# Kernel optimization log

Hardware: AMD Instinct MI355X
Metric: run time of the kernel (lower is better)

The kernel has to match this reference:

```python
import math
import jax, jax.numpy as jnp
import numpy as np

NUM_CLASSES = 15
GAUSSIAN_FACTOR = 12.0
SCORE_THRESHOLD = 0.23
EPS = 1e-9
IMG = 1024
STRIDES = [8, 16, 32, 64, 128]
REGRESS_RANGES = [(-1.0, 64.0), (64.0, 128.0), (128.0, 256.0), (256.0, 512.0), (512.0, 1e8)]
NUM_ANCHORS_PER_LEVEL = [(IMG // s) ** 2 for s in STRIDES]
RANGES_PER_ANCHOR = np.concatenate(
    [np.tile(np.array(r, np.float32), (n, 1)) for r, n in zip(REGRESS_RANGES, NUM_ANCHORS_PER_LEVEL)], axis=0)


def rbox_to_poly(rb):
    # rb: (..., 5) [cx, cy, w, h, angle] -> (..., 4, 2) corners
    cx, cy, w, h, ang = (rb[..., 0], rb[..., 1], rb[..., 2], rb[..., 3], rb[..., 4])
    cxs = jnp.stack([-w / 2, w / 2, w / 2, -w / 2], axis=-1)
    cys = jnp.stack([-h / 2, -h / 2, h / 2, h / 2], axis=-1)
    ca = jnp.cos(ang)[..., None]
    sa = jnp.sin(ang)[..., None]
    px = cxs * ca - cys * sa + cx[..., None]
    py = cxs * sa + cys * ca + cy[..., None]
    return jnp.stack([px, py], axis=-1)


def rbox_to_gauss(rb):
    # rbox -> 2D gaussian (mean, covariance entries a, b, c)
    x, y, w, h, a = (rb[..., 0], rb[..., 1], rb[..., 2], rb[..., 3], rb[..., 4])
    ca, sa = jnp.cos(a), jnp.sin(a)
    w2, h2 = w * w / 12.0, h * h / 12.0
    return x, y, w2 * ca * ca + h2 * sa * sa, w2 * sa * sa + h2 * ca * ca, (w2 - h2) * ca * sa


def probiou(box1, box2, eps=1e-3):
    # ProbIoU between rotated boxes via Bhattacharyya distance of gaussians
    x1, y1, a1, b1, c1 = rbox_to_gauss(box1)
    x2, y2, a2, b2, c2 = rbox_to_gauss(box2)
    dx, dy = x1 - x2, y1 - y2
    aa, bb, cc = a1 + a2, b1 + b2, c1 + c2
    denom = aa * bb - cc * cc + eps
    t1 = 0.25 * (aa * dy * dy + bb * dx * dx) / denom
    t2 = 0.5 * (cc * (-dx) * dy) / denom
    det1 = jnp.maximum(a1 * b1 - c1 * c1, 0.0)
    det2 = jnp.maximum(a2 * b2 - c2 * c2, 0.0)
    t3 = 0.5 * jnp.log(denom / (4.0 * jnp.sqrt(det1 * det2) + eps) + eps)
    bd = jnp.clip(t1 + t2 + t3, eps, 100.0)
    return 1.0 - jnp.sqrt(1.0 - jnp.exp(-bd) + eps)


def _forward(pred_scores, pred_boxes, anchor_points, gt_labels, gt_boxes, pad_gt_mask, bg_index, stride_tensor):
    B, L, C = pred_scores.shape
    polys = rbox_to_poly(gt_boxes)                        # (B,N,4,2)
    a = polys[..., 0, :]
    b = polys[..., 1, :]
    d = polys[..., 3, :]
    vab = b - a                                           # (B,N,2)
    vad = d - a
    pts = anchor_points[None]                             # (1,1,L,2)
    # ---- gaussian distribution scores ----
    ctp = pts - gt_boxes[:, :, None, :2]                  # (B,N,L,2)
    dot_ab = jnp.sum(ctp * vab[:, :, None, :], -1)        # (B,N,L)
    dot_ad = jnp.sum(ctp * vad[:, :, None, :], -1)
    norm_ab = jnp.sqrt(jnp.sum(vab * vab, -1) + EPS)[:, :, None]
    norm_ad = jnp.sqrt(jnp.sum(vad * vad, -1) + EPS)[:, :, None]
    min_edge = jnp.min(gt_boxes[..., 2:4], -1)[:, :, None]
    delta_x = dot_ab ** 2 / (norm_ab ** 3 * min_edge + EPS)
    delta_y = dot_ad ** 2 / (norm_ad ** 3 * min_edge + EPS)
    gauss = jnp.exp(-0.5 * GAUSSIAN_FACTOR * (delta_x + delta_y))
    sigma = min_edge / GAUSSIAN_FACTOR
    refined = gauss / (2.0 * math.pi * sigma + EPS)
    # ---- geometric constraints: inside rotated polygon AND score > threshold ----
    ap = pts - a[:, :, None, :]                           # (B,N,L,2)
    ap_ab = jnp.sum(ap * vab[:, :, None, :], -1)
    ap_ad = jnp.sum(ap * vad[:, :, None, :], -1)
    nab2 = jnp.sum(vab * vab, -1)[:, :, None]
    nad2 = jnp.sum(vad * vad, -1)[:, :, None]
    inside = (ap_ab >= EPS) & (ap_ab <= nab2) & (ap_ad >= EPS) & (ap_ad <= nad2)
    inside_mask = (inside & (gauss > SCORE_THRESHOLD)).astype(pred_scores.dtype)
    # ---- multi-level range constraint on axis-aligned hull ----
    cx, cy, w, h, ang = (gt_boxes[..., i] for i in range(5))
    ca, sa = jnp.abs(jnp.cos(ang)), jnp.abs(jnp.sin(ang))
    ew = 0.5 * (w * ca + h * sa)
    eh = 0.5 * (w * sa + h * ca)
    x1y1 = jnp.stack([cx - ew, cy - eh], -1)[:, :, None, :]
    x2y2 = jnp.stack([cx + ew, cy + eh], -1)[:, :, None, :]
    ltrb_max = jnp.maximum(jnp.max(pts - x1y1, -1), jnp.max(x2y2 - pts, -1))  # (B,N,L)
    rr = jnp.asarray(RANGES_PER_ANCHOR)                   # (L,2)
    low = rr[None, None, :, 0]
    high = rr[None, None, :, 1]
    range_mask = ((ltrb_max >= low) & (ltrb_max <= high)).astype(pred_scores.dtype)
    # ---- combine masks and select best GT per anchor ----
    positive_mask = inside_mask * range_mask * pad_gt_mask  # (B,N,L), pad (B,N,1)
    masked = refined * positive_mask - (1.0 - positive_mask)
    best_idx = jnp.argmax(masked, axis=1)                 # (B,L)
    best_score = jnp.max(masked, axis=1)
    pos = best_score > 0.0
    lbl = jnp.take_along_axis(gt_labels[..., 0], best_idx, axis=1)
    assigned_labels = jnp.where(pos, lbl, bg_index)
    gb = jnp.take_along_axis(gt_boxes, best_idx[..., None], axis=1)  # (B,L,5)
    assigned_boxes = jnp.where(pos[..., None], gb, 0.0)
    # ---- IoU-weighted one-hot quality scores ----
    oh = jax.nn.one_hot(assigned_labels, NUM_CLASSES + 1, dtype=pred_scores.dtype)
    oh = jnp.delete(oh, bg_index, axis=-1)                # drop background column
    iou = jnp.where(pos, probiou(pred_boxes, gb), 0.0)
    assigned_scores = oh * iou[..., None]
    return assigned_labels, assigned_boxes, assigned_scores


def setup_inputs() -> dict:
    key = jax.random.key(0)
    ks = jax.random.split(key, 6)
    pts, strides = [], []
    for s in STRIDES:
        n = IMG // s
        xs = (np.arange(n, dtype=np.float32) + 0.5) * s
        gy, gx = np.meshgrid(xs, xs, indexing='ij')
        pts.append(np.stack([gx.ravel(), gy.ravel()], -1))
        strides.append(np.full((n * n, 1), float(s), np.float32))
    anchor_points = jnp.asarray(np.concatenate(pts, 0))[None]       # (1,L,2)
    stride_tensor = jnp.asarray(np.concatenate(strides, 0))[None]   # (1,L,1)
    L = anchor_points.shape[1]
    B, N, C = 8, 64, NUM_CLASSES

    def rand_rboxes(k, shape):
        k1, k2, k3 = jax.random.split(k, 3)
        cxy = jax.random.uniform(k1, shape[:-1] + (2,), minval=0.0, maxval=float(IMG))
        wh = jax.random.uniform(k2, shape[:-1] + (2,), minval=16.0, maxval=256.0)
        ang = jax.random.uniform(k3, shape[:-1] + (1,), minval=-np.pi / 2, maxval=np.pi / 2)
        return jnp.concatenate([cxy, wh, ang], -1).astype(jnp.float32)

    return {
        'pred_scores': jax.nn.sigmoid(jax.random.normal(ks[0], (B, L, C), jnp.float32)),
        'pred_boxes': rand_rboxes(ks[1], (B, L, 5)),
        'anchor_points': anchor_points,
        'gt_labels': jax.random.randint(ks[2], (B, N, 1), 0, C),
        'gt_boxes': rand_rboxes(ks[3], (B, N, 5)),
        'pad_gt_mask': jnp.ones((B, N, 1), jnp.float32),
        'bg_index': C,
        'stride_tensor': stride_tensor,
    }


def reference(pred_scores, pred_boxes, anchor_points, gt_labels, gt_boxes, pad_gt_mask, bg_index, stride_tensor):
    return _forward(pred_scores, pred_boxes, anchor_points, gt_labels, gt_boxes, pad_gt_mask, bg_index, stride_tensor)
```

## Files before the change

### kernel.cpp

```cpp
#include <hip/hip_runtime.h>
#include <math.h>


#define NUMC 15
#define NGT  64
#define LTOT 21824
#define NB   8
#define EPSV 1e-9f
#define SCORE_THR 0.23f

__global__ __launch_bounds__(256) void rga_main(
    const float* __restrict__ pred_boxes,
    const float* __restrict__ anchor_points,
    const int*   __restrict__ gt_labels,
    const float* __restrict__ gt_boxes,
    const float* __restrict__ pad_gt_mask,
    const int*   __restrict__ bg_index_p,
    float* __restrict__ out)
{
    __shared__ float4 SA[NGT][5];
    __shared__ float4 SE[NGT][2];

    const int b   = blockIdx.y;
    const int tid = threadIdx.x;

    if (tid < NGT) {
        const float* g = gt_boxes + (size_t)(b * NGT + tid) * 5;
        const float cx = g[0], cy = g[1], w = g[2], h = g[3], ang = g[4];
        const float ca = cosf(ang), sa = sinf(ang);
        const float hw = 0.5f * w, hh = 0.5f * h;
        const float ax = (-hw) * ca - (-hh) * sa + cx;
        const float ay = (-hw) * sa + (-hh) * ca + cy;
        const float bx = ( hw) * ca - (-hh) * sa + cx;
        const float by = ( hw) * sa + (-hh) * ca + cy;
        const float dx_ = (-hw) * ca - ( hh) * sa + cx;
        const float dy_ = (-hw) * sa + ( hh) * ca + cy;
        const float vabx = bx - ax, vaby = by - ay;
        const float vadx = dx_ - ax, vady = dy_ - ay;
        const float nab2 = vabx * vabx + vaby * vaby;
        const float nad2 = vadx * vadx + vady * vady;
        const float norm_ab = sqrtf(nab2 + EPSV);
        const float norm_ad = sqrtf(nad2 + EPSV);
        const float min_edge = fminf(w, h);
        const float inv_dxden = 1.0f / (norm_ab * norm_ab * norm_ab * min_edge + EPSV);
        const float inv_dyden = 1.0f / (norm_ad * norm_ad * norm_ad * min_edge + EPSV);
        const float sigma = min_edge / 12.0f;
        const float inv_refden = 1.0f / (6.2831853071795864769f * sigma + EPSV);
        const float aca = fabsf(ca), asa = fabsf(sa);
        const float ew = 0.5f * (w * aca + h * asa);
        const float eh = 0.5f * (w * asa + h * aca);
        const float w2 = w * w / 12.0f, h2 = h * h / 12.0f;
        const float ga2 = w2 * ca * ca + h2 * sa * sa;
        const float gb2 = w2 * sa * sa + h2 * ca * ca;
        const float gc2 = (w2 - h2) * ca * sa;
        const float det2 = fmaxf(ga2 * gb2 - gc2 * gc2, 0.0f);
        const float labelf = (float)gt_labels[b * NGT + tid];
        const float pad    = pad_gt_mask[b * NGT + tid];

        SA[tid][0] = make_float4(cx, cy, ax, ay);
        SA[tid][1] = make_float4(vabx, vaby, vadx, vady);
        SA[tid][2] = make_float4(nab2, nad2, inv_dxden, inv_dyden);
        SA[tid][3] = make_float4(cx - ew, cy - eh, cx + ew, cy + eh);
        SA[tid][4] = make_float4(inv_refden, pad, labelf, 0.0f);
        SE[tid][0] = make_float4(w, h, ang, det2);
        SE[tid][1] = make_float4(ga2, gb2, gc2, 0.0f);
    }
    __syncthreads();

    const int l = blockIdx.x * blockDim.x + tid;
    if (l >= LTOT) return;

    const float2 p = ((const float2*)anchor_points)[l];
    const float px = p.x, py = p.y;

    float low, high;
    if (l < 16384)      { low = -1.0f;   high = 64.0f;  }
    else if (l < 20480) { low = 64.0f;   high = 128.0f; }
    else if (l < 21504) { low = 128.0f;  high = 256.0f; }
    else if (l < 21760) { low = 256.0f;  high = 512.0f; }
    else                { low = 512.0f;  high = 1e8f;   }

    float best = -2.0f;
    int   bidx = 0;
    #pragma unroll 4
    for (int n = 0; n < NGT; ++n) {
        const float4 f0 = SA[n][0];
        const float4 f1 = SA[n][1];
        const float4 f2 = SA[n][2];
        const float4 f3 = SA[n][3];
        const float4 f4 = SA[n][4];
        const float ctpx = px - f0.x, ctpy = py - f0.y;
        const float dot_ab = ctpx * f1.x + ctpy * f1.y;
        const float dot_ad = ctpx * f1.z + ctpy * f1.w;
        const float delta = dot_ab * dot_ab * f2.z + dot_ad * dot_ad * f2.w;
        const float gauss = expf(-6.0f * delta);
        const float apx = px - f0.z, apy = py - f0.w;
        const float ap_ab = apx * f1.x + apy * f1.y;
        const float ap_ad = apx * f1.z + apy * f1.w;
        const bool inside = (ap_ab >= EPSV) & (ap_ab <= f2.x) &
                            (ap_ad >= EPSV) & (ap_ad <= f2.y);
        const float ltrb = fmaxf(fmaxf(px - f3.x, py - f3.y),
                                 fmaxf(f3.z - px, f3.w - py));
        const bool ok = inside & (gauss > SCORE_THR) & (ltrb >= low) & (ltrb <= high);
        const float mask = ok ? f4.y : 0.0f;
        const float masked = gauss * f4.x * mask - (1.0f - mask);
        if (masked > best) { best = masked; bidx = n; }
    }

    const int bg = bg_index_p[0];
    const bool pos = best > 0.0f;

    const float4 s0 = SA[bidx][0];
    const float4 s4 = SA[bidx][4];
    const float4 e0 = SE[bidx][0];
    const float4 e1 = SE[bidx][1];

    const int lbl = pos ? (int)s4.z : bg;

    const size_t idx = (size_t)b * LTOT + l;
    out[idx] = (float)lbl;

    float* outB = out + (size_t)NB * LTOT + idx * 5;
    outB[0] = pos ? s0.x : 0.0f;
    outB[1] = pos ? s0.y : 0.0f;
    outB[2] = pos ? e0.x : 0.0f;
    outB[3] = pos ? e0.y : 0.0f;
    outB[4] = pos ? e0.z : 0.0f;

    float iou = 0.0f;
    if (pos) {
        const float* pb = pred_boxes + idx * 5;
        const float pcx = pb[0], pcy = pb[1], pw = pb[2], ph = pb[3], pang = pb[4];
        const float ca = cosf(pang), sa = sinf(pang);
        const float w2 = pw * pw / 12.0f, h2 = ph * ph / 12.0f;
        const float a1 = w2 * ca * ca + h2 * sa * sa;
        const float b1 = w2 * sa * sa + h2 * ca * ca;
        const float c1 = (w2 - h2) * ca * sa;
        const float dx = pcx - s0.x, dy = pcy - s0.y;
        const float aa = a1 + e1.x, bb = b1 + e1.y, cc = c1 + e1.z;
        const float denom = aa * bb - cc * cc + 1e-3f;
        const float t1 = 0.25f * (aa * dy * dy + bb * dx * dx) / denom;
        const float t2 = 0.5f * (cc * (-(dx * dy))) / denom;
        const float det1 = fmaxf(a1 * b1 - c1 * c1, 0.0f);
        const float t3 = 0.5f * logf(denom / (4.0f * sqrtf(det1 * e0.w) + 1e-3f) + 1e-3f);
        float bd = t1 + t2 + t3;
        bd = fminf(fmaxf(bd, 1e-3f), 100.0f);
        iou = 1.0f - sqrtf(1.0f - expf(-bd) + 1e-3f);
    }

    float* outS = out + (size_t)NB * LTOT * 6 + idx * NUMC;
    #pragma unroll
    for (int c = 0; c < NUMC; ++c)
        outS[c] = (pos && c == lbl) ? iou : 0.0f;
}

extern "C" void kernel_launch(void* const* d_in, const int* in_sizes, int n_in,
                              void* d_out, int out_size, void* d_ws, size_t ws_size,
                              hipStream_t stream) {
    const float* pred_boxes    = (const float*)d_in[1];
    const float* anchor_points = (const float*)d_in[2];
    const int*   gt_labels     = (const int*)d_in[3];
    const float* gt_boxes      = (const float*)d_in[4];
    const float* pad_gt_mask   = (const float*)d_in[5];
    const int*   bg_index_p    = (const int*)d_in[6];
    float*       out           = (float*)d_out;

    dim3 grid((LTOT + 255) / 256, NB);
    rga_main<<<grid, dim3(256), 0, stream>>>(
        pred_boxes, anchor_points, gt_labels, gt_boxes, pad_gt_mask, bg_index_p, out);
}
```

Before: 96.74 us.

## Precompute GT box features in separate kernel; read via uniform global loads

Moves the per-GT-box feature precomputation into a separate single-block prep kernel that writes to workspace. The main kernel now reads those features through uniform global (scalar-cacheable) loads instead of shared memory, which removes the per-block trig prologue and the block barrier. It also simplifies the masked-score expression with a fused multiply-add and switches to fast-math intrinsics for exp, log and trig. The trade-off is an extra kernel launch, plus small accuracy changes from the intrinsics.

```diff
diff --git a/kernel.cpp b/kernel.cpp
--- a/kernel.cpp
+++ b/kernel.cpp
@@ -9,65 +9,66 @@
 #define EPSV 1e-9f
 #define SCORE_THR 0.23f
 
+
+__global__ __launch_bounds__(512) void rga_prep(
+    const float* __restrict__ gt_boxes,
+    const int*   __restrict__ gt_labels,
+    const float* __restrict__ pad_gt_mask,
+    float4* __restrict__ W)
+{
+    const int t = threadIdx.x;
+    if (t >= NB * NGT) return;
+    const float* g = gt_boxes + (size_t)t * 5;
+    const float cx = g[0], cy = g[1], w = g[2], h = g[3], ang = g[4];
+    const float ca = cosf(ang), sa = sinf(ang);
+    const float hw = 0.5f * w, hh = 0.5f * h;
+    const float ax = (-hw) * ca - (-hh) * sa + cx;
+    const float ay = (-hw) * sa + (-hh) * ca + cy;
+    const float bx = ( hw) * ca - (-hh) * sa + cx;
+    const float by = ( hw) * sa + (-hh) * ca + cy;
+    const float dx_ = (-hw) * ca - ( hh) * sa + cx;
+    const float dy_ = (-hw) * sa + ( hh) * ca + cy;
+    const float vabx = bx - ax, vaby = by - ay;
+    const float vadx = dx_ - ax, vady = dy_ - ay;
+    const float nab2 = vabx * vabx + vaby * vaby;
+    const float nad2 = vadx * vadx + vady * vady;
+    const float norm_ab = sqrtf(nab2 + EPSV);
+    const float norm_ad = sqrtf(nad2 + EPSV);
+    const float min_edge = fminf(w, h);
+    const float inv_dxden = 1.0f / (norm_ab * norm_ab * norm_ab * min_edge + EPSV);
+    const float inv_dyden = 1.0f / (norm_ad * norm_ad * norm_ad * min_edge + EPSV);
+    const float sigma = min_edge / 12.0f;
+    const float inv_refden = 1.0f / (6.2831853071795864769f * sigma + EPSV);
+    const float aca = fabsf(ca), asa = fabsf(sa);
+    const float ew = 0.5f * (w * aca + h * asa);
+    const float eh = 0.5f * (w * asa + h * aca);
+    const float w2 = w * w / 12.0f, h2 = h * h / 12.0f;
+    const float ga2 = w2 * ca * ca + h2 * sa * sa;
+    const float gb2 = w2 * sa * sa + h2 * ca * ca;
+    const float gc2 = (w2 - h2) * ca * sa;
+    const float det2 = fmaxf(ga2 * gb2 - gc2 * gc2, 0.0f);
+    const float pad = pad_gt_mask[t];
+    const float labelf = (float)gt_labels[t];
+
+    float4* o = W + (size_t)t * 7;
+    o[0] = make_float4(cx, cy, ax, ay);
+    o[1] = make_float4(vabx, vaby, vadx, vady);
+    o[2] = make_float4(nab2, nad2, inv_dxden, inv_dyden);
+    o[3] = make_float4(cx - ew, cy - eh, cx + ew, cy + eh);
+    o[4] = make_float4(inv_refden * pad, pad - 1.0f, labelf, 0.0f);
+    o[5] = make_float4(w, h, ang, det2);
+    o[6] = make_float4(ga2, gb2, gc2, 0.0f);
+}
+
 __global__ __launch_bounds__(256) void rga_main(
-    const float* __restrict__ pred_boxes,
-    const float* __restrict__ anchor_points,
-    const int*   __restrict__ gt_labels,
-    const float* __restrict__ gt_boxes,
-    const float* __restrict__ pad_gt_mask,
-    const int*   __restrict__ bg_index_p,
+    const float*  __restrict__ pred_boxes,
+    const float*  __restrict__ anchor_points,
+    const int*    __restrict__ bg_index_p,
+    const float4* __restrict__ W,
     float* __restrict__ out)
 {
-    __shared__ float4 SA[NGT][5];
-    __shared__ float4 SE[NGT][2];
-
-    const int b   = blockIdx.y;
-    const int tid = threadIdx.x;
-
-    if (tid < NGT) {
-        const float* g = gt_boxes + (size_t)(b * NGT + tid) * 5;
-        const float cx = g[0], cy = g[1], w = g[2], h = g[3], ang = g[4];
-        const float ca = cosf(ang), sa = sinf(ang);
-        const float hw = 0.5f * w, hh = 0.5f * h;
-        const float ax = (-hw) * ca - (-hh) * sa + cx;
-        const float ay = (-hw) * sa + (-hh) * ca + cy;
-        const float bx = ( hw) * ca - (-hh) * sa + cx;
-        const float by = ( hw) * sa + (-hh) * ca + cy;
-        const float dx_ = (-hw) * ca - ( hh) * sa + cx;
-        const float dy_ = (-hw) * sa + ( hh) * ca + cy;
-        const float vabx = bx - ax, vaby = by - ay;
-        const float vadx = dx_ - ax, vady = dy_ - ay;
-        const float nab2 = vabx * vabx + vaby * vaby;
-        const float nad2 = vadx * vadx + vady * vady;
-        const float norm_ab = sqrtf(nab2 + EPSV);
-        const float norm_ad = sqrtf(nad2 + EPSV);
-        const float min_edge = fminf(w, h);
-        const float inv_dxden = 1.0f / (norm_ab * norm_ab * norm_ab * min_edge + EPSV);
-        const float inv_dyden = 1.0f / (norm_ad * norm_ad * norm_ad * min_edge + EPSV);
-        const float sigma = min_edge / 12.0f;
-        const float inv_refden = 1.0f / (6.2831853071795864769f * sigma + EPSV);
-        const float aca = fabsf(ca), asa = fabsf(sa);
-        const float ew = 0.5f * (w * aca + h * asa);
-        const float eh = 0.5f * (w * asa + h * aca);
-        const float w2 = w * w / 12.0f, h2 = h * h / 12.0f;
-        const float ga2 = w2 * ca * ca + h2 * sa * sa;
-        const float gb2 = w2 * sa * sa + h2 * ca * ca;
-        const float gc2 = (w2 - h2) * ca * sa;
-        const float det2 = fmaxf(ga2 * gb2 - gc2 * gc2, 0.0f);
-        const float labelf = (float)gt_labels[b * NGT + tid];
-        const float pad    = pad_gt_mask[b * NGT + tid];
-
-        SA[tid][0] = make_float4(cx, cy, ax, ay);
-        SA[tid][1] = make_float4(vabx, vaby, vadx, vady);
-        SA[tid][2] = make_float4(nab2, nad2, inv_dxden, inv_dyden);
-        SA[tid][3] = make_float4(cx - ew, cy - eh, cx + ew, cy + eh);
-        SA[tid][4] = make_float4(inv_refden, pad, labelf, 0.0f);
-        SE[tid][0] = make_float4(w, h, ang, det2);
-        SE[tid][1] = make_float4(ga2, gb2, gc2, 0.0f);
-    }
-    __syncthreads();
-
-    const int l = blockIdx.x * blockDim.x + tid;
+    const int b = blockIdx.y;
+    const int l = blockIdx.x * blockDim.x + threadIdx.x;
     if (l >= LTOT) return;
 
     const float2 p = ((const float2*)anchor_points)[l];
@@ -80,20 +81,22 @@
     else if (l < 21760) { low = 256.0f;  high = 512.0f; }
     else                { low = 512.0f;  high = 1e8f;   }
 
+    const float4* __restrict__ Pb = W + (size_t)b * NGT * 7;
+
     float best = -2.0f;
     int   bidx = 0;
-    #pragma unroll 4
+    #pragma unroll 2
     for (int n = 0; n < NGT; ++n) {
-        const float4 f0 = SA[n][0];
-        const float4 f1 = SA[n][1];
-        const float4 f2 = SA[n][2];
-        const float4 f3 = SA[n][3];
-        const float4 f4 = SA[n][4];
+        const float4 f0 = Pb[n * 7 + 0];
+        const float4 f1 = Pb[n * 7 + 1];
+        const float4 f2 = Pb[n * 7 + 2];
+        const float4 f3 = Pb[n * 7 + 3];
+        const float4 f4 = Pb[n * 7 + 4];
         const float ctpx = px - f0.x, ctpy = py - f0.y;
         const float dot_ab = ctpx * f1.x + ctpy * f1.y;
         const float dot_ad = ctpx * f1.z + ctpy * f1.w;
         const float delta = dot_ab * dot_ab * f2.z + dot_ad * dot_ad * f2.w;
-        const float gauss = expf(-6.0f * delta);
+        const float gauss = __expf(-6.0f * delta);
         const float apx = px - f0.z, apy = py - f0.w;
         const float ap_ab = apx * f1.x + apy * f1.y;
         const float ap_ad = apx * f1.z + apy * f1.w;
@@ -102,18 +105,18 @@
         const float ltrb = fmaxf(fmaxf(px - f3.x, py - f3.y),
                                  fmaxf(f3.z - px, f3.w - py));
         const bool ok = inside & (gauss > SCORE_THR) & (ltrb >= low) & (ltrb <= high);
-        const float mask = ok ? f4.y : 0.0f;
-        const float masked = gauss * f4.x * mask - (1.0f - mask);
+        const float masked = ok ? fmaf(gauss, f4.x, f4.y) : -1.0f;
         if (masked > best) { best = masked; bidx = n; }
     }
 
     const int bg = bg_index_p[0];
     const bool pos = best > 0.0f;
 
-    const float4 s0 = SA[bidx][0];
-    const float4 s4 = SA[bidx][4];
-    const float4 e0 = SE[bidx][0];
-    const float4 e1 = SE[bidx][1];
+    const float4* Wn = Pb + bidx * 7;
+    const float4 s0 = Wn[0];
+    const float4 s4 = Wn[4];
+    const float4 e0 = Wn[5];
+    const float4 e1 = Wn[6];
 
     const int lbl = pos ? (int)s4.z : bg;
 
@@ -131,7 +134,7 @@
     if (pos) {
         const float* pb = pred_boxes + idx * 5;
         const float pcx = pb[0], pcy = pb[1], pw = pb[2], ph = pb[3], pang = pb[4];
-        const float ca = cosf(pang), sa = sinf(pang);
+        const float ca = __cosf(pang), sa = __sinf(pang);
         const float w2 = pw * pw / 12.0f, h2 = ph * ph / 12.0f;
         const float a1 = w2 * ca * ca + h2 * sa * sa;
         const float b1 = w2 * sa * sa + h2 * ca * ca;
@@ -142,10 +145,10 @@
         const float t1 = 0.25f * (aa * dy * dy + bb * dx * dx) / denom;
         const float t2 = 0.5f * (cc * (-(dx * dy))) / denom;
         const float det1 = fmaxf(a1 * b1 - c1 * c1, 0.0f);
-        const float t3 = 0.5f * logf(denom / (4.0f * sqrtf(det1 * e0.w) + 1e-3f) + 1e-3f);
+        const float t3 = 0.5f * __logf(denom / (4.0f * __fsqrt_rn(det1 * e0.w) + 1e-3f) + 1e-3f);
         float bd = t1 + t2 + t3;
         bd = fminf(fmaxf(bd, 1e-3f), 100.0f);
-        iou = 1.0f - sqrtf(1.0f - expf(-bd) + 1e-3f);
+        iou = 1.0f - sqrtf(1.0f - __expf(-bd) + 1e-3f);
     }
 
     float* outS = out + (size_t)NB * LTOT * 6 + idx * NUMC;
@@ -164,8 +167,11 @@
     const float* pad_gt_mask   = (const float*)d_in[5];
     const int*   bg_index_p    = (const int*)d_in[6];
     float*       out           = (float*)d_out;
+    float4*      W             = (float4*)d_ws;
+
+    rga_prep<<<dim3(1), dim3(512), 0, stream>>>(gt_boxes, gt_labels, pad_gt_mask, W);
 
     dim3 grid((LTOT + 255) / 256, NB);
     rga_main<<<grid, dim3(256), 0, stream>>>(
-        pred_boxes, anchor_points, gt_labels, gt_boxes, pad_gt_mask, bg_index_p, out);
+        pred_boxes, anchor_points, bg_index_p, W, out);
 }
```

Measured after the change: 98.39 us. About the same (+1.7%).

## Cull GT boxes per block by spatial and range overlap before anchor loop

Applied to the files above, without the earlier changes.

Each block derives its pyramid level and row span from its block index, then builds a compacted list of GT boxes whose axis-aligned extent and size could match anchors in that tile. Only those boxes are scanned per anchor, which skips most of the 64-box loop. The change also switches to fast intrinsics (__expf, __sinf, __cosf, __logf) and folds the pad mask into a single fma. The risks are small numerical differences from the fast math and correctness depending on the culling margins being conservative.

```diff
diff --git a/kernel.cpp b/kernel.cpp
--- a/kernel.cpp
+++ b/kernel.cpp
@@ -8,8 +8,9 @@
 #define NB   8
 #define EPSV 1e-9f
 #define SCORE_THR 0.23f
-
-__global__ __launch_bounds__(256) void rga_main(
+#define MARG 2.0f
+
+__global__ __launch_bounds__(256) void rga_fused(
     const float* __restrict__ pred_boxes,
     const float* __restrict__ anchor_points,
     const int*   __restrict__ gt_labels,
@@ -20,22 +21,43 @@
 {
     __shared__ float4 SA[NGT][5];
     __shared__ float4 SE[NGT][2];
+    __shared__ int    keep_list[NGT];
+    __shared__ int    keep_cnt;
 
     const int b   = blockIdx.y;
+    const int bx  = blockIdx.x;
     const int tid = threadIdx.x;
 
+    int Ls, sgn, log2nc;
+    float low, high;
+    if (bx < 64)      { Ls = 0;     sgn = 8;   log2nc = 7; low = -1.0f;  high = 64.0f;  }
+    else if (bx < 80) { Ls = 16384; sgn = 16;  log2nc = 6; low = 64.0f;  high = 128.0f; }
+    else if (bx < 84) { Ls = 20480; sgn = 32;  log2nc = 5; low = 128.0f; high = 256.0f; }
+    else if (bx < 85) { Ls = 21504; sgn = 64;  log2nc = 4; low = 256.0f; high = 512.0f; }
+    else              { Ls = 21760; sgn = 128; log2nc = 3; low = 512.0f; high = 1e8f;   }
+    const int   nc     = 1 << log2nc;
+    const int   row0   = (bx * 256 - Ls) >> log2nc;
+    const int   nrows  = 256 >> log2nc;
+    const int   rowlast = min(row0 + nrows, nc) - 1;
+    const float fs     = (float)sgn;
+    const float bymin  = (row0 + 0.5f) * fs;
+    const float bymax  = (rowlast + 0.5f) * fs;
+    const float bxmin  = 0.5f * fs;
+    const float bxmax  = (nc - 0.5f) * fs;
+
     if (tid < NGT) {
-        const float* g = gt_boxes + (size_t)(b * NGT + tid) * 5;
+        const int gi = b * NGT + tid;
+        const float* g = gt_boxes + (size_t)gi * 5;
         const float cx = g[0], cy = g[1], w = g[2], h = g[3], ang = g[4];
         const float ca = cosf(ang), sa = sinf(ang);
         const float hw = 0.5f * w, hh = 0.5f * h;
         const float ax = (-hw) * ca - (-hh) * sa + cx;
         const float ay = (-hw) * sa + (-hh) * ca + cy;
-        const float bx = ( hw) * ca - (-hh) * sa + cx;
-        const float by = ( hw) * sa + (-hh) * ca + cy;
+        const float bx_ = ( hw) * ca - (-hh) * sa + cx;
+        const float by_ = ( hw) * sa + (-hh) * ca + cy;
         const float dx_ = (-hw) * ca - ( hh) * sa + cx;
         const float dy_ = (-hw) * sa + ( hh) * ca + cy;
-        const float vabx = bx - ax, vaby = by - ay;
+        const float vabx = bx_ - ax, vaby = by_ - ay;
         const float vadx = dx_ - ax, vady = dy_ - ay;
         const float nab2 = vabx * vabx + vaby * vaby;
         const float nad2 = vadx * vadx + vady * vady;
@@ -54,36 +76,44 @@
         const float gb2 = w2 * sa * sa + h2 * ca * ca;
         const float gc2 = (w2 - h2) * ca * sa;
         const float det2 = fmaxf(ga2 * gb2 - gc2 * gc2, 0.0f);
-        const float labelf = (float)gt_labels[b * NGT + tid];
-        const float pad    = pad_gt_mask[b * NGT + tid];
+        const float pad = pad_gt_mask[gi];
+        const float labelf = (float)gt_labels[gi];
+        const float x1 = cx - ew, y1 = cy - eh, x2 = cx + ew, y2 = cy + eh;
 
         SA[tid][0] = make_float4(cx, cy, ax, ay);
         SA[tid][1] = make_float4(vabx, vaby, vadx, vady);
         SA[tid][2] = make_float4(nab2, nad2, inv_dxden, inv_dyden);
-        SA[tid][3] = make_float4(cx - ew, cy - eh, cx + ew, cy + eh);
-        SA[tid][4] = make_float4(inv_refden, pad, labelf, 0.0f);
+        SA[tid][3] = make_float4(x1, y1, x2, y2);
+        SA[tid][4] = make_float4(inv_refden * pad, pad - 1.0f, labelf, 0.0f);
         SE[tid][0] = make_float4(w, h, ang, det2);
         SE[tid][1] = make_float4(ga2, gb2, gc2, 0.0f);
+
+        const float me = fmaxf(ew, eh);
+        const bool keep =
+            (x1 <= bxmax + MARG) && (x2 >= bxmin - MARG) &&
+            (y1 <= bymax + MARG) && (y2 >= bymin - MARG) &&
+            (me <= high + MARG) && (2.0f * me >= low - MARG) &&
+            (pad > 0.0f);
+        const unsigned long long bal = __ballot(keep);
+        const int lane = tid & 63;
+        const int pos_i = (int)__popcll(bal & ((1ULL << lane) - 1ULL));
+        if (keep) keep_list[pos_i] = tid;
+        if (lane == 0) keep_cnt = (int)__popcll(bal);
     }
     __syncthreads();
 
-    const int l = blockIdx.x * blockDim.x + tid;
-    if (l >= LTOT) return;
+    const int cnt = keep_cnt;
+    const int l_raw = bx * 256 + tid;
+    if (l_raw >= LTOT) return;
+    const int l = l_raw;
 
     const float2 p = ((const float2*)anchor_points)[l];
     const float px = p.x, py = p.y;
 
-    float low, high;
-    if (l < 16384)      { low = -1.0f;   high = 64.0f;  }
-    else if (l < 20480) { low = 64.0f;   high = 128.0f; }
-    else if (l < 21504) { low = 128.0f;  high = 256.0f; }
-    else if (l < 21760) { low = 256.0f;  high = 512.0f; }
-    else                { low = 512.0f;  high = 1e8f;   }
-
     float best = -2.0f;
     int   bidx = 0;
-    #pragma unroll 4
-    for (int n = 0; n < NGT; ++n) {
+    for (int i = 0; i < cnt; ++i) {
+        const int n = keep_list[i];
         const float4 f0 = SA[n][0];
         const float4 f1 = SA[n][1];
         const float4 f2 = SA[n][2];
@@ -93,7 +123,7 @@
         const float dot_ab = ctpx * f1.x + ctpy * f1.y;
         const float dot_ad = ctpx * f1.z + ctpy * f1.w;
         const float delta = dot_ab * dot_ab * f2.z + dot_ad * dot_ad * f2.w;
-        const float gauss = expf(-6.0f * delta);
+        const float gauss = __expf(-6.0f * delta);
         const float apx = px - f0.z, apy = py - f0.w;
         const float ap_ab = apx * f1.x + apy * f1.y;
         const float ap_ad = apx * f1.z + apy * f1.w;
@@ -102,8 +132,7 @@
         const float ltrb = fmaxf(fmaxf(px - f3.x, py - f3.y),
                                  fmaxf(f3.z - px, f3.w - py));
         const bool ok = inside & (gauss > SCORE_THR) & (ltrb >= low) & (ltrb <= high);
-        const float mask = ok ? f4.y : 0.0f;
-        const float masked = gauss * f4.x * mask - (1.0f - mask);
+        const float masked = ok ? fmaf(gauss, f4.x, f4.y) : -1.0f;
         if (masked > best) { best = masked; bidx = n; }
     }
 
@@ -131,7 +160,7 @@
     if (pos) {
         const float* pb = pred_boxes + idx * 5;
         const float pcx = pb[0], pcy = pb[1], pw = pb[2], ph = pb[3], pang = pb[4];
-        const float ca = cosf(pang), sa = sinf(pang);
+        const float ca = __cosf(pang), sa = __sinf(pang);
         const float w2 = pw * pw / 12.0f, h2 = ph * ph / 12.0f;
         const float a1 = w2 * ca * ca + h2 * sa * sa;
         const float b1 = w2 * sa * sa + h2 * ca * ca;
@@ -142,10 +171,10 @@
         const float t1 = 0.25f * (aa * dy * dy + bb * dx * dx) / denom;
         const float t2 = 0.5f * (cc * (-(dx * dy))) / denom;
         const float det1 = fmaxf(a1 * b1 - c1 * c1, 0.0f);
-        const float t3 = 0.5f * logf(denom / (4.0f * sqrtf(det1 * e0.w) + 1e-3f) + 1e-3f);
+        const float t3 = 0.5f * __logf(denom / (4.0f * __fsqrt_rn(det1 * e0.w) + 1e-3f) + 1e-3f);
         float bd = t1 + t2 + t3;
         bd = fminf(fmaxf(bd, 1e-3f), 100.0f);
-        iou = 1.0f - sqrtf(1.0f - expf(-bd) + 1e-3f);
+        iou = 1.0f - sqrtf(1.0f - __expf(-bd) + 1e-3f);
     }
 
     float* outS = out + (size_t)NB * LTOT * 6 + idx * NUMC;
@@ -166,6 +195,6 @@
     float*       out           = (float*)d_out;
 
     dim3 grid((LTOT + 255) / 256, NB);
-    rga_main<<<grid, dim3(256), 0, stream>>>(
+    rga_fused<<<grid, dim3(256), 0, stream>>>(
         pred_boxes, anchor_points, gt_labels, gt_boxes, pad_gt_mask, bg_index_p, out);
 }
```

Result: faster. 83.45 us (-13.7%).
